# Performance work log

Measured on AMD Instinct MI355X. Metric: run time of the kernel, lower is better.

The kernel has to match this reference:

```python
import math
import jax, jax.numpy as jnp
import numpy as np

N, C, H, W, G = 32, 128, 56, 56, 32
SHIFT = 1  # fixed value for random.randint(-1, 1) chosen at module init


def _unfold_h(x):
    # F.unfold(x, (3,1), dilation=(2,1), padding=(2,0)) -> (n, c, 3, h, w)
    p = jnp.pad(x, ((0, 0), (0, 0), (2, 2), (0, 0)))
    return jnp.stack([p[:, :, 0:H], p[:, :, 2:H + 2], p[:, :, 4:H + 4]], axis=2)


def _unfold_w(x):
    # F.unfold(x, (1,3), dilation=(1,2), padding=(0,2)) -> (n, c, 3, h, w)
    p = jnp.pad(x, ((0, 0), (0, 0), (0, 0), (2, 2)))
    return jnp.stack([p[:, :, :, 0:W], p[:, :, :, 2:W + 2], p[:, :, :, 4:W + 4]], axis=2)


def setup_inputs() -> dict:
    key = jax.random.key(0)
    k1, k2, k3, k4 = jax.random.split(key, 4)
    x = jax.random.normal(k1, (N, C, H, W), dtype=jnp.float32)
    p2w = jax.random.normal(k2, (1, C, 3, H, W), dtype=jnp.float32) * 0.02
    p5w = jax.random.normal(k3, (1, C, 1, 1), dtype=jnp.float32) * 0.02
    conv_w = jax.random.normal(k4, (C // G, C), dtype=jnp.float32) * 0.02  # 1x1 conv, no bias
    return {"x": x, "p2w": p2w, "p5w": p5w, "conv_w": conv_w}


def reference(x, p2w, p5w, conv_w):
    n = x.shape[0]
    t1 = _unfold_h(x)                      # (n, c, 3, h, w)
    t2 = p2w * t1                          # (n, c, 3, h, w)
    t3 = _unfold_w(x)                      # (n, c, 3, h, w)
    t4 = jnp.roll(x, SHIFT, axis=2)        # roll along height
    t5 = p5w * t4
    t6 = t4 + x
    t2f = t2.reshape(n, C * 3, H * W)
    t6f = t6.reshape(n, C, H * W)
    # bmm: (n, c*3, hw) x (n, hw, c) -> (n, c*3, c)
    t7 = jnp.einsum('nkp,ncp->nkc', t2f, t6f) / math.sqrt(H * W)
    # 1x1 conv: (c//g, c) applied pointwise
    t8 = jnp.einsum('oc,nchw->nohw', conv_w, t5)            # (n, c//g, h, w)
    t9 = (t8[:, None] * x.reshape(n, G, C // G, H, W)).reshape(n, C, H, W)
    t3f = t3.reshape(n, C * 3, H * W)
    # bmm: (n, c, c*3) x (n, c*3, hw) -> (n, c, hw)
    t10 = (jnp.einsum('nkc,nkp->ncp', t7, t3f) / math.sqrt(C * 3)).reshape(n, C, H, W)
    return t9 + t10
```

## Files before the change

kernel.cpp:

```cpp
#include <hip/hip_runtime.h>

#define NB 32
#define CCH 128
#define HH 56
#define WWD 56
#define HWP (HH*WWD)
#define K3C (3*CCH)
#define SPLITK 8

typedef _Float16 half8 __attribute__((ext_vector_type(8)));
typedef float floatx4 __attribute__((ext_vector_type(4)));

__global__ __launch_bounds__(256) void prep_kernel(const float* __restrict__ x,
                                                   const float* __restrict__ p2w,
                                                   _Float16* __restrict__ xh,
                                                   _Float16* __restrict__ xT,
                                                   _Float16* __restrict__ p2wh) {
    __shared__ _Float16 t[64 * 72];
    const int bid = blockIdx.x;
    const int tid = threadIdx.x;

    if (bid >= 3136) {
        const int row = bid - 3136;
        const int j = row >> 7;
        const int c = row & 127;
        const float* s = p2w + ((size_t)c * 3 + j) * HWP;
        _Float16* d = p2wh + (size_t)row * HWP;
        for (int base = tid * 8; base < HWP; base += 2048) {
            const float4 a = *(const float4*)(s + base);
            const float4 b = *(const float4*)(s + base + 4);
            half8 v;
            v[0] = (_Float16)a.x; v[1] = (_Float16)a.y; v[2] = (_Float16)a.z; v[3] = (_Float16)a.w;
            v[4] = (_Float16)b.x; v[5] = (_Float16)b.y; v[6] = (_Float16)b.z; v[7] = (_Float16)b.w;
            *(half8*)(d + base) = v;
        }
        return;
    }

    const int r8  = bid & 7;
    const int g   = bid >> 3;
    const int n   = r8 + 8 * (g / 98);
    const int rem = g % 98;
    const int c0  = (rem / 49) * 64;
    const int p0  = (rem % 49) * 64;
    const int r   = tid >> 2;
    const int seg = (tid & 3) * 16;

    const float* src = x + ((size_t)n * CCH + c0 + r) * HWP + p0 + seg;
    const float4 a0 = *(const float4*)(src);
    const float4 a1 = *(const float4*)(src + 4);
    const float4 a2 = *(const float4*)(src + 8);
    const float4 a3 = *(const float4*)(src + 12);
    half8 v0, v1;
    v0[0] = (_Float16)a0.x; v0[1] = (_Float16)a0.y; v0[2] = (_Float16)a0.z; v0[3] = (_Float16)a0.w;
    v0[4] = (_Float16)a1.x; v0[5] = (_Float16)a1.y; v0[6] = (_Float16)a1.z; v0[7] = (_Float16)a1.w;
    v1[0] = (_Float16)a2.x; v1[1] = (_Float16)a2.y; v1[2] = (_Float16)a2.z; v1[3] = (_Float16)a2.w;
    v1[4] = (_Float16)a3.x; v1[5] = (_Float16)a3.y; v1[6] = (_Float16)a3.z; v1[7] = (_Float16)a3.w;

    _Float16* dxh = xh + ((size_t)n * CCH + c0 + r) * HWP + p0 + seg;
    *(half8*)(dxh)     = v0;
    *(half8*)(dxh + 8) = v1;
    *(half8*)(&t[r * 72 + seg])     = v0;
    *(half8*)(&t[r * 72 + seg + 8]) = v1;
    __syncthreads();
    _Float16* dst = xT + ((size_t)n * HWP + p0 + r) * CCH + c0 + seg;
    half8 w0, w1;
#pragma unroll
    for (int i = 0; i < 8; ++i) w0[i] = t[(seg + i) * 72 + r];
#pragma unroll
    for (int i = 0; i < 8; ++i) w1[i] = t[(seg + 8 + i) * 72 + r];
    *(half8*)(dst) = w0;
    *(half8*)(dst + 8) = w1;
}

__global__ __launch_bounds__(256) void gemm1_kernel(const _Float16* __restrict__ xh,
                                                    const _Float16* __restrict__ p2wh,
                                                    _Float16* __restrict__ part) {
    __shared__ _Float16 As[128 * 72];
    __shared__ _Float16 Bs[128 * 72];

    const int bid   = blockIdx.x;
    const int r8    = bid & 7;
    const int g     = bid >> 3;
    const int n     = r8 + 8 * (g / 24);
    const int inner = g % 24;
    const int jb    = inner % 3;
    const int m0    = jb * 128;
    const int s     = inner / 3;
    const int i0    = (s * 49) >> 3;
    const int i1    = ((s + 1) * 49) >> 3;

    const int tid  = threadIdx.x;
    const int lrow = tid >> 3;
    const int lcol = (tid & 7) * 8;

    const int ashift = 112 * (jb - 1);
    const _Float16* xh_n = xh + (size_t)n * CCH * HWP;
    const _Float16* pw_m = p2wh + (size_t)m0 * HWP;

    const int wave = tid >> 6;
    const int lane = tid & 63;
    const int l15  = lane & 15;
    const int quad = lane >> 4;
    const int wm   = (wave >> 1) * 64;
    const int wn   = (wave & 1) * 64;

    floatx4 acc[4][4];
#pragma unroll
    for (int a = 0; a < 4; ++a)
#pragma unroll
        for (int b = 0; b < 4; ++b) acc[a][b] = (floatx4){0.f,0.f,0.f,0.f};

    half8 xv[4], wv[4], uv[4], vv[4];

    {
        const int p0 = i0 * 64;
        const int pA = p0 + lcol;
        const int srcp  = pA + ashift;
        const int proll = (pA >= WWD) ? (pA - WWD) : (pA + (HH - 1) * WWD);
        const bool ok = (srcp >= 0 && srcp < HWP);
#pragma unroll
        for (int sg = 0; sg < 4; ++sg) {
            const int row = sg * 32 + lrow;
            const _Float16* xaS = xh_n + (size_t)row * HWP;
            if (ok) xv[sg] = *(const half8*)(xaS + srcp);
            else { half8 z; for (int i = 0; i < 8; ++i) z[i] = (_Float16)0.f; xv[sg] = z; }
            wv[sg] = *(const half8*)(pw_m + (size_t)row * HWP + pA);
            uv[sg] = *(const half8*)(xaS + pA);
            vv[sg] = *(const half8*)(xaS + proll);
        }
    }

    for (int it = i0; it < i1; ++it) {
#pragma unroll
        for (int sg = 0; sg < 4; ++sg) {
            const int row = sg * 32 + lrow;
            *(half8*)(&As[row * 72 + lcol]) = xv[sg] * wv[sg];
            *(half8*)(&Bs[row * 72 + lcol]) = uv[sg] + vv[sg];
        }
        __syncthreads();
        if (it + 1 < i1) {
            const int p0 = (it + 1) * 64;
            const int pA = p0 + lcol;
            const int srcp  = pA + ashift;
            const int proll = (pA >= WWD) ? (pA - WWD) : (pA + (HH - 1) * WWD);
            const bool ok = (srcp >= 0 && srcp < HWP);
#pragma unroll
            for (int sg = 0; sg < 4; ++sg) {
                const int row = sg * 32 + lrow;
                const _Float16* xaS = xh_n + (size_t)row * HWP;
                if (ok) xv[sg] = *(const half8*)(xaS + srcp);
                else { half8 z; for (int i = 0; i < 8; ++i) z[i] = (_Float16)0.f; xv[sg] = z; }
                wv[sg] = *(const half8*)(pw_m + (size_t)row * HWP + pA);
                uv[sg] = *(const half8*)(xaS + pA);
                vv[sg] = *(const half8*)(xaS + proll);
            }
        }
#pragma unroll
        for (int ks = 0; ks < 2; ++ks) {
            const int ko = ks * 32 + quad * 8;
            half8 af[4], bf[4];
#pragma unroll
            for (int mi = 0; mi < 4; ++mi) af[mi] = *(half8*)(&As[(wm + mi * 16 + l15) * 72 + ko]);
#pragma unroll
            for (int ni = 0; ni < 4; ++ni) bf[ni] = *(half8*)(&Bs[(wn + ni * 16 + l15) * 72 + ko]);
#pragma unroll
            for (int mi = 0; mi < 4; ++mi)
#pragma unroll
                for (int ni = 0; ni < 4; ++ni)
                    acc[mi][ni] = __builtin_amdgcn_mfma_f32_16x16x32_f16(af[mi], bf[ni], acc[mi][ni], 0, 0, 0);
        }
        __syncthreads();
    }

    _Float16* pbase = part + (size_t)(s * NB + n) * K3C * CCH;
#pragma unroll
    for (int mi = 0; mi < 4; ++mi)
#pragma unroll
        for (int ni = 0; ni < 4; ++ni) {
            const int kr = m0 + wm + mi * 16 + quad * 4;
            const int cc = wn + ni * 16 + l15;
#pragma unroll
            for (int r2 = 0; r2 < 4; ++r2)
                pbase[(size_t)(kr + r2) * CCH + cc] = (_Float16)acc[mi][ni][r2];
        }
}

__global__ __launch_bounds__(256) void reduce_kernel(const _Float16* __restrict__ part,
                                                     _Float16* __restrict__ t7T) {
    __shared__ _Float16 tile[16][130];
    const int n  = blockIdx.y;
    const int k0 = blockIdx.x * 16;
    const int t  = threadIdx.x;
    const int c2 = t & 127;
    const int kh = t >> 7;
#pragma unroll
    for (int kk = 0; kk < 8; ++kk) {
        const int k = kh * 8 + kk;
        float sum = 0.f;
#pragma unroll
        for (int sp = 0; sp < SPLITK; ++sp)
            sum += (float)part[(((size_t)sp * NB + n) * K3C + k0 + k) * CCH + c2];
        tile[k][c2] = (_Float16)(sum * (1.0f / 56.0f));
    }
    __syncthreads();
    const int kt = t & 15;
    const int c0 = t >> 4;
#pragma unroll
    for (int cc = 0; cc < 8; ++cc) {
        const int cw = c0 * 8 + cc;
        t7T[((size_t)n * CCH + cw) * K3C + k0 + kt] = tile[kt][cw];
    }
}

__global__ __launch_bounds__(256) void gemm2_kernel(const _Float16* __restrict__ xh,
                                                    const _Float16* __restrict__ xT,
                                                    const _Float16* __restrict__ t7T,
                                                    const float* __restrict__ conv_w,
                                                    const float* __restrict__ p5w,
                                                    float* __restrict__ out) {
    __shared__ _Float16 As[128 * 72];
    __shared__ _Float16 Bs[64 * 72];
    __shared__ float t8tile[4 * 64];
    __shared__ float wf[4 * 128];

    const int bid = blockIdx.x;
    const int r8  = bid & 7;
    const int g   = bid >> 3;
    const int n   = r8 + 8 * (g / 49);
    const int pt0 = (g % 49) * 64;
    const int tid = threadIdx.x;

    const int lrow = tid >> 3;
    const int lcol = (tid & 7) * 8;

    const _Float16* t7n = t7T + (size_t)n * CCH * K3C;
    const _Float16* xTn = xT + (size_t)n * HWP * CCH;

    int hbArr[2], wbArr[2];
#pragma unroll
    for (int sg = 0; sg < 2; ++sg) {
        const int prow = pt0 + sg * 32 + lrow;
        hbArr[sg] = prow / WWD;
        wbArr[sg] = prow - hbArr[sg] * WWD;
    }

    const int wave = tid >> 6;
    const int lane = tid & 63;
    const int l15  = lane & 15;
    const int quad = lane >> 4;
    const int wm   = (wave >> 1) * 64;
    const int wn   = (wave & 1) * 32;

    floatx4 acc[4][2];
#pragma unroll
    for (int a = 0; a < 4; ++a)
#pragma unroll
        for (int b = 0; b < 2; ++b) acc[a][b] = (floatx4){0.f,0.f,0.f,0.f};

    half8 avA[4], bvA[2], avB[4], bvB[2];

    auto issue2 = [&](int kn, half8 (&av)[4], half8 (&bv)[2]) {
        const int jn  = kn >> 7;
        const int c0k = kn & 127;
#pragma unroll
        for (int sg = 0; sg < 4; ++sg)
            av[sg] = *(const half8*)(t7n + (size_t)(sg * 32 + lrow) * K3C + kn + lcol);
#pragma unroll
        for (int sg = 0; sg < 2; ++sg) {
            const int wsrc = wbArr[sg] + 2 * jn - 2;
            if (wsrc >= 0 && wsrc < WWD) {
                bv[sg] = *(const half8*)(xTn + ((size_t)hbArr[sg] * WWD + wsrc) * CCH + c0k + lcol);
            } else {
                half8 z; for (int i = 0; i < 8; ++i) z[i] = (_Float16)0.f; bv[sg] = z;
            }
        }
    };
    auto commit2 = [&](half8 (&av)[4], half8 (&bv)[2]) {
#pragma unroll
        for (int sg = 0; sg < 4; ++sg)
            *(half8*)(&As[(sg * 32 + lrow) * 72 + lcol]) = av[sg];
#pragma unroll
        for (int sg = 0; sg < 2; ++sg)
            *(half8*)(&Bs[(sg * 32 + lrow) * 72 + lcol]) = bv[sg];
    };

    issue2(0, avA, bvA);
    issue2(64, avB, bvB);

    {
        wf[tid]       = conv_w[tid] * p5w[tid & 127];
        wf[tid + 256] = conv_w[tid + 256] * p5w[tid & 127];
        _Float16* tr = As;
        const int coff = (tid & 15) * 8;
#pragma unroll
        for (int q = 0; q < 4; ++q) {
            const int row = q * 16 + (tid >> 4);
            const int p   = pt0 + row;
            const int srcrow = (p >= WWD) ? (p - WWD) : (p + (HH - 1) * WWD);
            *(half8*)(&tr[row * 136 + coff]) = *(const half8*)(xTn + (size_t)srcrow * CCH + coff);
        }
        __syncthreads();
        const int o  = tid >> 6;
        const int pl = tid & 63;
        const float* wrow = wf + o * 128;
        float a = 0.f;
#pragma unroll
        for (int cs = 0; cs < 16; ++cs) {
            const half8 v = *(const half8*)(&tr[pl * 136 + cs * 8]);
#pragma unroll
            for (int i = 0; i < 8; ++i) a += wrow[cs * 8 + i] * (float)v[i];
        }
        t8tile[o * 64 + pl] = a;
        __syncthreads();
    }

#pragma unroll
    for (int i = 0; i < 6; ++i) {
        if ((i & 1) == 0) commit2(avA, bvA); else commit2(avB, bvB);
        __syncthreads();
        if (i + 2 < 6) {
            if ((i & 1) == 0) issue2((i + 2) * 64, avA, bvA);
            else              issue2((i + 2) * 64, avB, bvB);
        }
#pragma unroll
        for (int ks = 0; ks < 2; ++ks) {
            const int ko = ks * 32 + quad * 8;
            half8 af[4], bf[2];
#pragma unroll
            for (int mi = 0; mi < 4; ++mi) af[mi] = *(half8*)(&As[(wm + mi * 16 + l15) * 72 + ko]);
#pragma unroll
            for (int ni = 0; ni < 2; ++ni) bf[ni] = *(half8*)(&Bs[(wn + ni * 16 + l15) * 72 + ko]);
#pragma unroll
            for (int mi = 0; mi < 4; ++mi)
#pragma unroll
                for (int ni = 0; ni < 2; ++ni)
                    acc[mi][ni] = __builtin_amdgcn_mfma_f32_16x16x32_f16(af[mi], bf[ni], acc[mi][ni], 0, 0, 0);
        }
        __syncthreads();
    }

    const float sc = 0.05103103630798288f;
#pragma unroll
    for (int mi = 0; mi < 4; ++mi)
#pragma unroll
        for (int ni = 0; ni < 2; ++ni) {
            const int ccb = wm + mi * 16 + quad * 4;
            const int lp  = wn + ni * 16 + l15;
            const int pp  = pt0 + lp;
#pragma unroll
            for (int r2 = 0; r2 < 4; ++r2) {
                const int c2 = ccb + r2;
                const size_t oidx = ((size_t)n * CCH + c2) * HWP + pp;
                const float t9 = t8tile[r2 * 64 + lp] * (float)xh[oidx];
                out[oidx] = acc[mi][ni][r2] * sc + t9;
            }
        }
}

extern "C" void kernel_launch(void* const* d_in, const int* in_sizes, int n_in,
                              void* d_out, int out_size, void* d_ws, size_t ws_size,
                              hipStream_t stream) {
    const float* x      = (const float*)d_in[0];
    const float* p2w    = (const float*)d_in[1];
    const float* p5w    = (const float*)d_in[2];
    const float* conv_w = (const float*)d_in[3];
    float* out = (float*)d_out;

    char* ws = (char*)d_ws;
    _Float16* xh   = (_Float16*)ws;
    _Float16* p2wh = (_Float16*)(ws + 25690112);
    _Float16* t7T  = (_Float16*)(ws + 25690112 + 2408448 + 1605632);
    _Float16* xT   = (_Float16*)(ws + 25690112 + 2408448 + 1605632 + 3145728);
    _Float16* part = (_Float16*)out;

    prep_kernel<<<dim3(3520), dim3(256), 0, stream>>>(x, p2w, xh, xT, p2wh);
    gemm1_kernel<<<dim3(768), dim3(256), 0, stream>>>(xh, p2wh, part);
    reduce_kernel<<<dim3(24, NB), dim3(256), 0, stream>>>(part, t7T);
    gemm2_kernel<<<dim3(1568), dim3(256), 0, stream>>>(xh, xT, t7T, conv_w, p5w, out);
}
```

Baseline: 181.3 us.

## Stage GEMM epilogues through LDS for coalesced vector stores and simplify reduce

```diff
diff --git a/kernel.cpp b/kernel.cpp
--- a/kernel.cpp
+++ b/kernel.cpp
@@ -9,6 +9,7 @@
 #define SPLITK 8
 
 typedef _Float16 half8 __attribute__((ext_vector_type(8)));
+typedef _Float16 half4 __attribute__((ext_vector_type(4)));
 typedef float floatx4 __attribute__((ext_vector_type(4)));
 
 __global__ __launch_bounds__(256) void prep_kernel(const float* __restrict__ x,
@@ -76,8 +77,9 @@
 __global__ __launch_bounds__(256) void gemm1_kernel(const _Float16* __restrict__ xh,
                                                     const _Float16* __restrict__ p2wh,
                                                     _Float16* __restrict__ part) {
-    __shared__ _Float16 As[128 * 72];
-    __shared__ _Float16 Bs[128 * 72];
+    __shared__ _Float16 lds[2 * 128 * 72];
+    _Float16* As = lds;
+    _Float16* Bs = lds + 128 * 72;
 
     const int bid   = blockIdx.x;
     const int r8    = bid & 7;
@@ -173,44 +175,44 @@
         __syncthreads();
     }
 
-    _Float16* pbase = part + (size_t)(s * NB + n) * K3C * CCH;
+    _Float16* ct = lds;
 #pragma unroll
     for (int mi = 0; mi < 4; ++mi)
 #pragma unroll
         for (int ni = 0; ni < 4; ++ni) {
-            const int kr = m0 + wm + mi * 16 + quad * 4;
+            const int kr = wm + mi * 16 + quad * 4;
             const int cc = wn + ni * 16 + l15;
-#pragma unroll
-            for (int r2 = 0; r2 < 4; ++r2)
-                pbase[(size_t)(kr + r2) * CCH + cc] = (_Float16)acc[mi][ni][r2];
-        }
+            half4 pk;
+#pragma unroll
+            for (int r2 = 0; r2 < 4; ++r2) pk[r2] = (_Float16)acc[mi][ni][r2];
+            *(half4*)(&ct[cc * 136 + kr]) = pk;
+        }
+    __syncthreads();
+    {
+        const int cc = tid >> 1;
+        const int ks = (tid & 1) * 64;
+        _Float16* pb = part + ((size_t)(s * NB + n) * CCH + cc) * K3C + m0 + ks;
+#pragma unroll
+        for (int j = 0; j < 8; ++j)
+            *(half8*)(pb + j * 8) = *(const half8*)(&ct[cc * 136 + ks + j * 8]);
+    }
 }
 
 __global__ __launch_bounds__(256) void reduce_kernel(const _Float16* __restrict__ part,
                                                      _Float16* __restrict__ t7T) {
-    __shared__ _Float16 tile[16][130];
-    const int n  = blockIdx.y;
-    const int k0 = blockIdx.x * 16;
-    const int t  = threadIdx.x;
-    const int c2 = t & 127;
-    const int kh = t >> 7;
-#pragma unroll
-    for (int kk = 0; kk < 8; ++kk) {
-        const int k = kh * 8 + kk;
-        float sum = 0.f;
-#pragma unroll
-        for (int sp = 0; sp < SPLITK; ++sp)
-            sum += (float)part[(((size_t)sp * NB + n) * K3C + k0 + k) * CCH + c2];
-        tile[k][c2] = (_Float16)(sum * (1.0f / 56.0f));
-    }
-    __syncthreads();
-    const int kt = t & 15;
-    const int c0 = t >> 4;
-#pragma unroll
-    for (int cc = 0; cc < 8; ++cc) {
-        const int cw = c0 * 8 + cc;
-        t7T[((size_t)n * CCH + cw) * K3C + k0 + kt] = tile[kt][cw];
-    }
+    const size_t slab = (size_t)NB * CCH * K3C;
+    const size_t i = ((size_t)blockIdx.x * 256 + threadIdx.x) * 8;
+    float sum[8] = {0.f,0.f,0.f,0.f,0.f,0.f,0.f,0.f};
+#pragma unroll
+    for (int sp = 0; sp < SPLITK; ++sp) {
+        const half8 v = *(const half8*)(part + sp * slab + i);
+#pragma unroll
+        for (int j = 0; j < 8; ++j) sum[j] += (float)v[j];
+    }
+    half8 o;
+#pragma unroll
+    for (int j = 0; j < 8; ++j) o[j] = (_Float16)(sum[j] * (1.0f / 56.0f));
+    *(half8*)(t7T + i) = o;
 }
 
 __global__ __launch_bounds__(256) void gemm2_kernel(const _Float16* __restrict__ xh,
@@ -341,21 +343,49 @@
     }
 
     const float sc = 0.05103103630798288f;
-#pragma unroll
-    for (int mi = 0; mi < 4; ++mi)
-#pragma unroll
-        for (int ni = 0; ni < 2; ++ni) {
-            const int ccb = wm + mi * 16 + quad * 4;
-            const int lp  = wn + ni * 16 + l15;
-            const int pp  = pt0 + lp;
-#pragma unroll
-            for (int r2 = 0; r2 < 4; ++r2) {
-                const int c2 = ccb + r2;
-                const size_t oidx = ((size_t)n * CCH + c2) * HWP + pp;
-                const float t9 = t8tile[r2 * 64 + lp] * (float)xh[oidx];
-                out[oidx] = acc[mi][ni][r2] * sc + t9;
+    float* st = (float*)As;
+    const int erow = tid >> 2;
+    const int eseg = (tid & 3) * 16;
+#pragma unroll
+    for (int h = 0; h < 2; ++h) {
+        if ((wave >> 1) == h) {
+#pragma unroll
+            for (int mi = 0; mi < 4; ++mi)
+#pragma unroll
+                for (int ni = 0; ni < 2; ++ni) {
+                    const int r0 = mi * 16 + quad * 4;
+                    const int cl = wn + ni * 16 + l15;
+#pragma unroll
+                    for (int r2 = 0; r2 < 4; ++r2)
+                        st[(r0 + r2) * 68 + cl] = acc[mi][ni][r2];
+                }
+        }
+        __syncthreads();
+        {
+            const int c2 = h * 64 + erow;
+            const size_t obase = ((size_t)n * CCH + c2) * HWP + pt0 + eseg;
+            const half8 x0 = *(const half8*)(xh + obase);
+            const half8 x1 = *(const half8*)(xh + obase + 8);
+#pragma unroll
+            for (int q = 0; q < 4; ++q) {
+                const float4 a4 = *(const float4*)(&st[erow * 68 + eseg + q * 4]);
+                const float4 t4 = *(const float4*)(&t8tile[(erow & 3) * 64 + eseg + q * 4]);
+                float xvf[4];
+#pragma unroll
+                for (int k = 0; k < 4; ++k) {
+                    const int e = q * 4 + k;
+                    xvf[k] = (float)((e < 8) ? x0[e] : x1[e - 8]);
+                }
+                float4 o;
+                o.x = a4.x * sc + t4.x * xvf[0];
+                o.y = a4.y * sc + t4.y * xvf[1];
+                o.z = a4.z * sc + t4.z * xvf[2];
+                o.w = a4.w * sc + t4.w * xvf[3];
+                *(float4*)(out + obase + q * 4) = o;
             }
         }
+        __syncthreads();
+    }
 }
 
 extern "C" void kernel_launch(void* const* d_in, const int* in_sizes, int n_in,
@@ -376,6 +406,6 @@
 
     prep_kernel<<<dim3(3520), dim3(256), 0, stream>>>(x, p2w, xh, xT, p2wh);
     gemm1_kernel<<<dim3(768), dim3(256), 0, stream>>>(xh, p2wh, part);
-    reduce_kernel<<<dim3(24, NB), dim3(256), 0, stream>>>(part, t7T);
+    reduce_kernel<<<dim3(768), dim3(256), 0, stream>>>(part, t7T);
     gemm2_kernel<<<dim3(1568), dim3(256), 0, stream>>>(xh, xT, t7T, conv_w, p5w, out);
 }
```

Result: slower. 190.6 us (+5.1%).

## Load gemm2 tiles directly into LDS with XOR-swizzled layout

Applied to the files above, without the earlier changes.

```diff
diff --git a/kernel.cpp b/kernel.cpp
--- a/kernel.cpp
+++ b/kernel.cpp
@@ -15,12 +15,14 @@
                                                    const float* __restrict__ p2w,
                                                    _Float16* __restrict__ xh,
                                                    _Float16* __restrict__ xT,
-                                                   _Float16* __restrict__ p2wh) {
+                                                   _Float16* __restrict__ p2wh,
+                                                   float* __restrict__ zbuf) {
     __shared__ _Float16 t[64 * 72];
     const int bid = blockIdx.x;
     const int tid = threadIdx.x;
 
     if (bid >= 3136) {
+        if (bid == 3136) zbuf[tid] = 0.f;
         const int row = bid - 3136;
         const int j = row >> 7;
         const int c = row & 127;
@@ -218,11 +220,13 @@
                                                     const _Float16* __restrict__ t7T,
                                                     const float* __restrict__ conv_w,
                                                     const float* __restrict__ p5w,
+                                                    const _Float16* __restrict__ zbuf,
                                                     float* __restrict__ out) {
-    __shared__ _Float16 As[128 * 72];
-    __shared__ _Float16 Bs[64 * 72];
+    __shared__ _Float16 lds[12800];
     __shared__ float t8tile[4 * 64];
     __shared__ float wf[4 * 128];
+    _Float16* As = lds;
+    _Float16* Bs = lds + 8704;
 
     const int bid = blockIdx.x;
     const int r8  = bid & 7;
@@ -231,20 +235,6 @@
     const int pt0 = (g % 49) * 64;
     const int tid = threadIdx.x;
 
-    const int lrow = tid >> 3;
-    const int lcol = (tid & 7) * 8;
-
-    const _Float16* t7n = t7T + (size_t)n * CCH * K3C;
-    const _Float16* xTn = xT + (size_t)n * HWP * CCH;
-
-    int hbArr[2], wbArr[2];
-#pragma unroll
-    for (int sg = 0; sg < 2; ++sg) {
-        const int prow = pt0 + sg * 32 + lrow;
-        hbArr[sg] = prow / WWD;
-        wbArr[sg] = prow - hbArr[sg] * WWD;
-    }
-
     const int wave = tid >> 6;
     const int lane = tid & 63;
     const int l15  = lane & 15;
@@ -252,46 +242,30 @@
     const int wm   = (wave >> 1) * 64;
     const int wn   = (wave & 1) * 32;
 
+    const int lr  = lane >> 3;
+    const int gcs = (lane & 7) ^ lr;
+
+    const _Float16* t7n = t7T + (size_t)n * CCH * K3C;
+    const _Float16* xTn = xT + (size_t)n * HWP * CCH;
+
+    int hbB[2], wbB[2];
+#pragma unroll
+    for (int cc = 0; cc < 2; ++cc) {
+        const int prow = pt0 + (wave * 2 + cc) * 8 + lr;
+        hbB[cc] = prow / WWD;
+        wbB[cc] = prow - hbB[cc] * WWD;
+    }
+
     floatx4 acc[4][2];
 #pragma unroll
     for (int a = 0; a < 4; ++a)
 #pragma unroll
         for (int b = 0; b < 2; ++b) acc[a][b] = (floatx4){0.f,0.f,0.f,0.f};
-
-    half8 avA[4], bvA[2], avB[4], bvB[2];
-
-    auto issue2 = [&](int kn, half8 (&av)[4], half8 (&bv)[2]) {
-        const int jn  = kn >> 7;
-        const int c0k = kn & 127;
-#pragma unroll
-        for (int sg = 0; sg < 4; ++sg)
-            av[sg] = *(const half8*)(t7n + (size_t)(sg * 32 + lrow) * K3C + kn + lcol);
-#pragma unroll
-        for (int sg = 0; sg < 2; ++sg) {
-            const int wsrc = wbArr[sg] + 2 * jn - 2;
-            if (wsrc >= 0 && wsrc < WWD) {
-                bv[sg] = *(const half8*)(xTn + ((size_t)hbArr[sg] * WWD + wsrc) * CCH + c0k + lcol);
-            } else {
-                half8 z; for (int i = 0; i < 8; ++i) z[i] = (_Float16)0.f; bv[sg] = z;
-            }
-        }
-    };
-    auto commit2 = [&](half8 (&av)[4], half8 (&bv)[2]) {
-#pragma unroll
-        for (int sg = 0; sg < 4; ++sg)
-            *(half8*)(&As[(sg * 32 + lrow) * 72 + lcol]) = av[sg];
-#pragma unroll
-        for (int sg = 0; sg < 2; ++sg)
-            *(half8*)(&Bs[(sg * 32 + lrow) * 72 + lcol]) = bv[sg];
-    };
-
-    issue2(0, avA, bvA);
-    issue2(64, avB, bvB);
 
     {
         wf[tid]       = conv_w[tid] * p5w[tid & 127];
         wf[tid + 256] = conv_w[tid + 256] * p5w[tid & 127];
-        _Float16* tr = As;
+        _Float16* tr = lds;
         const int coff = (tid & 15) * 8;
 #pragma unroll
         for (int q = 0; q < 4; ++q) {
@@ -315,22 +289,42 @@
         __syncthreads();
     }
 
-#pragma unroll
     for (int i = 0; i < 6; ++i) {
-        if ((i & 1) == 0) commit2(avA, bvA); else commit2(avB, bvB);
-        __syncthreads();
-        if (i + 2 < 6) {
-            if ((i & 1) == 0) issue2((i + 2) * 64, avA, bvA);
-            else              issue2((i + 2) * 64, avB, bvB);
-        }
+        const int kn  = i * 64;
+        const int jn  = i >> 1;
+        const int c0k = (i & 1) * 64;
+#pragma unroll
+        for (int cc = 0; cc < 4; ++cc) {
+            const int rowA = (wave * 4 + cc) * 8 + lr;
+            const _Float16* srcA = t7n + (size_t)rowA * K3C + kn + gcs * 8;
+            __builtin_amdgcn_global_load_lds(
+                (const __attribute__((address_space(1))) void*)srcA,
+                (__attribute__((address_space(3))) void*)(As + (wave * 4 + cc) * 512),
+                16, 0, 0);
+        }
+#pragma unroll
+        for (int cc = 0; cc < 2; ++cc) {
+            const int wsrc = wbB[cc] + 2 * jn - 2;
+            const _Float16* srcB = (wsrc >= 0 && wsrc < WWD)
+                ? xTn + ((size_t)hbB[cc] * WWD + wsrc) * CCH + c0k + gcs * 8
+                : zbuf + lane * 8;
+            __builtin_amdgcn_global_load_lds(
+                (const __attribute__((address_space(1))) void*)srcB,
+                (__attribute__((address_space(3))) void*)(Bs + (wave * 2 + cc) * 512),
+                16, 0, 0);
+        }
+        __syncthreads();
 #pragma unroll
         for (int ks = 0; ks < 2; ++ks) {
-            const int ko = ks * 32 + quad * 8;
+            const int ch = ks * 4 + quad;
+            const int sw = (ch ^ (l15 & 7)) * 8;
             half8 af[4], bf[2];
 #pragma unroll
-            for (int mi = 0; mi < 4; ++mi) af[mi] = *(half8*)(&As[(wm + mi * 16 + l15) * 72 + ko]);
-#pragma unroll
-            for (int ni = 0; ni < 2; ++ni) bf[ni] = *(half8*)(&Bs[(wn + ni * 16 + l15) * 72 + ko]);
+            for (int mi = 0; mi < 4; ++mi)
+                af[mi] = *(half8*)(&As[(wm + mi * 16 + l15) * 64 + sw]);
+#pragma unroll
+            for (int ni = 0; ni < 2; ++ni)
+                bf[ni] = *(half8*)(&Bs[(wn + ni * 16 + l15) * 64 + sw]);
 #pragma unroll
             for (int mi = 0; mi < 4; ++mi)
 #pragma unroll
@@ -370,12 +364,14 @@
     char* ws = (char*)d_ws;
     _Float16* xh   = (_Float16*)ws;
     _Float16* p2wh = (_Float16*)(ws + 25690112);
+    float*    zb   = (float*)   (ws + 25690112 + 2408448);
     _Float16* t7T  = (_Float16*)(ws + 25690112 + 2408448 + 1605632);
     _Float16* xT   = (_Float16*)(ws + 25690112 + 2408448 + 1605632 + 3145728);
     _Float16* part = (_Float16*)out;
 
-    prep_kernel<<<dim3(3520), dim3(256), 0, stream>>>(x, p2w, xh, xT, p2wh);
+    prep_kernel<<<dim3(3520), dim3(256), 0, stream>>>(x, p2w, xh, xT, p2wh, zb);
     gemm1_kernel<<<dim3(768), dim3(256), 0, stream>>>(xh, p2wh, part);
     reduce_kernel<<<dim3(24, NB), dim3(256), 0, stream>>>(part, t7T);
-    gemm2_kernel<<<dim3(1568), dim3(256), 0, stream>>>(xh, xT, t7T, conv_w, p5w, out);
-}
+    gemm2_kernel<<<dim3(1568), dim3(256), 0, stream>>>(xh, xT, t7T, conv_w, p5w,
+                                                       (const _Float16*)zb, out);
+}
```

Measured after the change: 194.9 us. 1.07x slower.
